# Kernel optimization log

Hardware: AMD Instinct MI355X
Metric: run time of the kernel (lower is better)

Reference implementation:

```python
import jax, jax.numpy as jnp
import numpy as np

TIME_DECAY = 0.1
B, S, D = 2048, 200, 128
H1, H2 = 64, 32


def setup_inputs() -> dict:
    key = jax.random.key(0)
    ks = jax.random.split(key, 8)
    query = jax.random.normal(ks[0], (B, D), dtype=jnp.float32)
    keys = jax.random.normal(ks[1], (B, S, D), dtype=jnp.float32)
    keys_mask = jax.random.randint(ks[2], (B, S), 0, 2).astype(jnp.bool_)
    # Linear weights stored as [in, out] (torch uses [out, in] with x @ W.T; same math)
    W1 = jax.random.normal(ks[3], (4 * D, H1), dtype=jnp.float32) / np.sqrt(4 * D)
    b1 = jnp.zeros((H1,), dtype=jnp.float32)
    a1 = jnp.asarray(0.25, dtype=jnp.float32)  # PReLU default init
    W2 = jax.random.normal(ks[4], (H1, H2), dtype=jnp.float32) / np.sqrt(H1)
    b2 = jnp.zeros((H2,), dtype=jnp.float32)
    a2 = jnp.asarray(0.25, dtype=jnp.float32)
    W3 = jax.random.normal(ks[5], (H2, 1), dtype=jnp.float32) / np.sqrt(H2)
    b3 = jnp.zeros((1,), dtype=jnp.float32)
    return {"query": query, "keys": keys, "keys_mask": keys_mask,
            "W1": W1, "b1": b1, "a1": a1, "W2": W2, "b2": b2, "a2": a2,
            "W3": W3, "b3": b3}


def _prelu(x, a):
    return jnp.maximum(x, 0) + a * jnp.minimum(x, 0)


def reference(query, keys, keys_mask, W1, b1, a1, W2, b2, a2, W3, b3):
    b, s, d = keys.shape
    q = jnp.broadcast_to(query[:, None, :], (b, s, d))
    # [B, S, 4D] concat of feature interactions
    x = jnp.concatenate([keys, q, keys * q, keys - q], axis=-1)
    h = _prelu(x @ W1 + b1, a1)
    h = _prelu(h @ W2 + b2, a2)
    scores = (h @ W3 + b3)[..., 0]  # [B, S]
    pos = jnp.arange(s, dtype=scores.dtype)
    time_w = jnp.exp(TIME_DECAY * (pos - s + 1))  # [S]
    scores = scores * time_w[None, :]
    scores = jnp.where(keys_mask, scores, -jnp.inf)
    w = jax.nn.softmax(scores, axis=-1)
    w = jnp.where(jnp.isnan(w), jnp.zeros_like(w), w)  # all-masked rows -> 0
    weighted_sum = jnp.einsum('bs,bsd->bd', w, keys)
    return weighted_sum, w
```

## Files before the change

### kernel.cpp

```cpp
#include <hip/hip_runtime.h>
#include <math.h>

#define NB 2048
#define NS 200
#define ND 128

typedef __attribute__((ext_vector_type(8))) short bf16x8;
typedef __attribute__((ext_vector_type(4))) float f32x4;
typedef __attribute__((ext_vector_type(4))) unsigned short u16x4;

#define U_W1HI  0
#define U_W1LO  4352
#define U_Q     8704
#define U_BIAS  8832
#define U_B2    8896
#define U_W3    8928
#define U_SC    8960
#define U_WB    9168
#define U_WRED  9376
#define U_BP    9384
#define U_TOTAL 9644

extern "C" __global__ void __launch_bounds__(256, 4)
tdra_main(const float* __restrict__ query,
          const float* __restrict__ keys,
          const int*   __restrict__ kmask,
          const float* __restrict__ W1,
          const float* __restrict__ b1,
          const float* __restrict__ a1p,
          const float* __restrict__ W2,
          const float* __restrict__ b2,
          const float* __restrict__ a2p,
          const float* __restrict__ W3,
          const float* __restrict__ b3p,
          float* __restrict__ out)
{
    __shared__ __align__(16) unsigned int smem[U_TOTAL];
    unsigned short* W1hi = (unsigned short*)(smem + U_W1HI);
    unsigned short* W1lo = (unsigned short*)(smem + U_W1LO);
    float* qf    = (float*)(smem + U_Q);
    float* biasE = (float*)(smem + U_BIAS);
    float* b2f   = (float*)(smem + U_B2);
    float* w3f   = (float*)(smem + U_W3);
    float* scf   = (float*)(smem + U_SC);
    float* wbf   = (float*)(smem + U_WB);
    float* wred  = (float*)(smem + U_WRED);
    float* bpf   = (float*)(smem + U_BP);

    const int tid = threadIdx.x;
    const int b   = blockIdx.x;
    const float a1 = a1p[0];
    const float a2 = a2p[0];
    const float b3 = b3p[0];

    const int wv = tid >> 6;
    const int c  = tid & 15;
    const int G  = (tid >> 4) & 3;

    if (tid < 32) {
        float4 qv = *(const float4*)(query + (size_t)b * ND + tid * 4);
        *(float4*)(qf + tid * 4) = qv;
    } else if (tid < 64) {
        b2f[tid - 32] = b2[tid - 32];
    } else if (tid < 96) {
        w3f[tid - 64] = W3[tid - 64];
    }

    bf16x8 A2h[2][2], A2l[2][2];
    #pragma unroll
    for (int jt = 0; jt < 2; ++jt)
        #pragma unroll
        for (int kt = 0; kt < 2; ++kt)
            #pragma unroll
            for (int e = 0; e < 8; ++e) {
                float x = W2[(kt * 32 + 8 * G + e) * 32 + jt * 16 + c];
                unsigned int u  = __float_as_uint(x);
                unsigned int hb = u & 0xFFFF0000u;
                float lof = x - __uint_as_float(hb);
                A2h[jt][kt][e] = (short)(u >> 16);
                A2l[jt][kt][e] = (short)(__float_as_uint(lof) >> 16);
            }
    __syncthreads();

    {
        int h = tid & 63, dg = tid >> 6;
        #pragma unroll 2
        for (int i = 0; i < 8; ++i) {
            int dblk = dg * 8 + i;
            u16x4 hi4, lo4;
            #pragma unroll
            for (int jj = 0; jj < 4; ++jj) {
                int d = dblk * 4 + jj;
                float qd = qf[d];
                float va = W1[d * 64 + h];
                float vc = W1[16384 + d * 64 + h];
                float vd = W1[24576 + d * 64 + h];
                float x  = va + vd + qd * vc;
                unsigned int u  = __float_as_uint(x);
                unsigned int hb = u & 0xFFFF0000u;
                float lof = x - __uint_as_float(hb);
                hi4[jj] = (unsigned short)(u >> 16);
                lo4[jj] = (unsigned short)(__float_as_uint(lof) >> 16);
            }
            *(u16x4*)(W1hi + h * 136 + dblk * 4) = hi4;
            *(u16x4*)(W1lo + h * 136 + dblk * 4) = lo4;
        }
        int qt = dg;
        const float* pb = W1 + (size_t)(128 + qt * 32) * 64 + h;
        const float* pd = W1 + (size_t)(384 + qt * 32) * 64 + h;
        float p = 0.f;
        #pragma unroll 8
        for (int i = 0; i < 32; ++i)
            p = fmaf(qf[qt * 32 + i], pb[i * 64] - pd[i * 64], p);
        bpf[qt * 65 + h] = p;
    }
    __syncthreads();
    if (tid < 64)
        biasE[tid] = b1[tid] + bpf[tid] + bpf[65 + tid] + bpf[130 + tid] + bpf[195 + tid];
    __syncthreads();

    #pragma unroll 1
    for (int st = wv; st < 13; st += 4) {
        int row = st * 16 + c; if (row > 199) row = 199;
        const float* kp = keys + ((size_t)b * NS + row) * ND + 8 * G;

        bf16x8 B1h[4], B1l[4];
        #pragma unroll
        for (int half = 0; half < 2; ++half) {
            float4 xs[4];
            #pragma unroll
            for (int q_ = 0; q_ < 2; ++q_) {
                xs[2 * q_]     = *(const float4*)(kp + (2 * half + q_) * 32);
                xs[2 * q_ + 1] = *(const float4*)(kp + (2 * half + q_) * 32 + 4);
            }
            #pragma unroll
            for (int q_ = 0; q_ < 2; ++q_) {
                int dt = 2 * half + q_;
                float t_[8] = {xs[2*q_].x, xs[2*q_].y, xs[2*q_].z, xs[2*q_].w,
                               xs[2*q_+1].x, xs[2*q_+1].y, xs[2*q_+1].z, xs[2*q_+1].w};
                #pragma unroll
                for (int e = 0; e < 8; ++e) {
                    unsigned int u  = __float_as_uint(t_[e]);
                    unsigned int hb = u & 0xFFFF0000u;
                    float lof = t_[e] - __uint_as_float(hb);
                    B1h[dt][e] = (short)(u >> 16);
                    B1l[dt][e] = (short)(__float_as_uint(lof) >> 16);
                }
            }
        }

        f32x4 acc1[4];
        #pragma unroll
        for (int ht = 0; ht < 4; ++ht)
            acc1[ht] = *(const f32x4*)(biasE + 16 * ht + 4 * G);
        #pragma unroll
        for (int dt = 0; dt < 4; ++dt) {
            #pragma unroll
            for (int ht = 0; ht < 4; ++ht) {
                int idx = (16 * ht + c) * 136 + 32 * dt + 8 * G;
                bf16x8 A1h = *(const bf16x8*)(W1hi + idx);
                bf16x8 A1l = *(const bf16x8*)(W1lo + idx);
                acc1[ht] = __builtin_amdgcn_mfma_f32_16x16x32_bf16(A1h, B1h[dt], acc1[ht], 0, 0, 0);
                acc1[ht] = __builtin_amdgcn_mfma_f32_16x16x32_bf16(A1h, B1l[dt], acc1[ht], 0, 0, 0);
                acc1[ht] = __builtin_amdgcn_mfma_f32_16x16x32_bf16(A1l, B1h[dt], acc1[ht], 0, 0, 0);
            }
        }

        unsigned int p[4][4];
        #pragma unroll
        for (int ht = 0; ht < 4; ++ht)
            #pragma unroll
            for (int r = 0; r < 4; ++r) {
                float v = acc1[ht][r];
                v = fmaxf(v, 0.f) + a1 * fminf(v, 0.f);
                unsigned int u  = __float_as_uint(v);
                unsigned int hb = u & 0xFFFF0000u;
                float lof = v - __uint_as_float(hb);
                p[ht][r] = (u >> 16) | (__float_as_uint(lof) & 0xFFFF0000u);
            }

        f32x4 acc2[2];
        acc2[0] = *(const f32x4*)(b2f + 4 * G);
        acc2[1] = *(const f32x4*)(b2f + 16 + 4 * G);
        const int srcbase = ((tid & 16) ? 32 : 0) + c;
        #pragma unroll
        for (int kt = 0; kt < 2; ++kt) {
            unsigned int q[8];
            #pragma unroll
            for (int half = 0; half < 2; ++half) {
                int src = srcbase + half * 16;
                #pragma unroll
                for (int r = 0; r < 4; ++r) {
                    unsigned int v0 = (unsigned int)__shfl((int)p[2 * kt][r], src, 64);
                    unsigned int v1 = (unsigned int)__shfl((int)p[2 * kt + 1][r], src, 64);
                    q[half * 4 + r] = (tid & 32) ? v1 : v0;
                }
            }
            bf16x8 B2h_, B2l_;
            #pragma unroll
            for (int e = 0; e < 8; ++e) {
                B2h_[e] = (short)(q[e] & 0xFFFFu);
                B2l_[e] = (short)(q[e] >> 16);
            }
            #pragma unroll
            for (int jt = 0; jt < 2; ++jt) {
                acc2[jt] = __builtin_amdgcn_mfma_f32_16x16x32_bf16(A2h[jt][kt], B2h_, acc2[jt], 0, 0, 0);
                acc2[jt] = __builtin_amdgcn_mfma_f32_16x16x32_bf16(A2h[jt][kt], B2l_, acc2[jt], 0, 0, 0);
                acc2[jt] = __builtin_amdgcn_mfma_f32_16x16x32_bf16(A2l[jt][kt], B2h_, acc2[jt], 0, 0, 0);
            }
        }

        float sv = 0.f;
        #pragma unroll
        for (int jt = 0; jt < 2; ++jt)
            #pragma unroll
            for (int r = 0; r < 4; ++r) {
                float v = acc2[jt][r];
                v = fmaxf(v, 0.f) + a2 * fminf(v, 0.f);
                sv = fmaf(v, w3f[jt * 16 + 4 * G + r], sv);
            }
        sv += __shfl_xor(sv, 16, 64);
        sv += __shfl_xor(sv, 32, 64);
        int srow = st * 16 + c;
        if ((tid & 48) == 0 && srow < NS) scf[srow] = sv + b3;
    }
    __syncthreads();

    float scval = -INFINITY;
    if (tid < NS) {
        if (kmask[(size_t)b * NS + tid] != 0)
            scval = scf[tid] * expf(0.1f * (float)(tid - (NS - 1)));
    }
    const int wid = tid >> 6, lane = tid & 63;
    float mx = scval;
    #pragma unroll
    for (int o = 32; o > 0; o >>= 1) mx = fmaxf(mx, __shfl_xor(mx, o, 64));
    if (lane == 0) wred[wid] = mx;
    __syncthreads();
    float M = fmaxf(fmaxf(wred[0], wred[1]), fmaxf(wred[2], wred[3]));
    float e = (M > -INFINITY) ? expf(scval - M) : 0.f;
    float ssum = e;
    #pragma unroll
    for (int o = 32; o > 0; o >>= 1) ssum += __shfl_xor(ssum, o, 64);
    if (lane == 0) wred[4 + wid] = ssum;
    __syncthreads();
    float SUM = wred[4] + wred[5] + wred[6] + wred[7];
    float wv_ = (SUM > 0.f) ? (e / SUM) : 0.f;
    if (tid < NS) {
        wbf[tid] = wv_;
        out[(size_t)NB * ND + (size_t)b * NS + tid] = wv_;
    }
    __syncthreads();

    {
        const int d = tid & 127, half = tid >> 7;
        const float* kp = keys + ((size_t)b * NS + half * 100) * ND + d;
        float pacc = 0.f;
        #pragma unroll 5
        for (int i = 0; i < 100; ++i)
            pacc = fmaf(wbf[half * 100 + i], kp[(size_t)i * ND], pacc);
        bpf[half * 128 + d] = pacc;
    }
    __syncthreads();
    if (tid < 128)
        out[(size_t)b * ND + tid] = bpf[tid] + bpf[128 + tid];
}

extern "C" void kernel_launch(void* const* d_in, const int* in_sizes, int n_in,
                              void* d_out, int out_size, void* d_ws, size_t ws_size,
                              hipStream_t stream) {
    (void)in_sizes; (void)n_in; (void)d_ws; (void)ws_size; (void)out_size;
    const float* query = (const float*)d_in[0];
    const float* keys  = (const float*)d_in[1];
    const int*   kmask = (const int*)d_in[2];
    const float* W1 = (const float*)d_in[3];
    const float* b1 = (const float*)d_in[4];
    const float* a1 = (const float*)d_in[5];
    const float* W2 = (const float*)d_in[6];
    const float* b2 = (const float*)d_in[7];
    const float* a2 = (const float*)d_in[8];
    const float* W3 = (const float*)d_in[9];
    const float* b3 = (const float*)d_in[10];
    float* out = (float*)d_out;

    hipLaunchKernelGGL(tdra_main, dim3(NB), dim3(256), 0, stream,
                       query, keys, kmask, W1, b1, a1, W2, b2, a2, W3, b3, out);
}
```

Before: 77.36 us.

## Fuse online softmax and weighted sum into the MLP tile loop

Computes the softmax with a running max and sum per thread, in the flash-attention style, and accumulates the weighted key sum from the key values already held in registers. This removes the second pass that reread all keys from global memory, along with the separate reduction barriers. The keys are rebuilt from their hi/lo bf16 split, and partial results are merged with cross-lane shuffles and then across waves. Each thread now keeps 32 extra accumulators, so the launch-bound occupancy hint drops from 4 to 3 blocks. The mask and time-decay factors are also precomputed into shared memory at the start.

Result: slower. 82.51 us (+6.6%).

```diff
diff --git a/kernel.cpp b/kernel.cpp
--- a/kernel.cpp
+++ b/kernel.cpp
@@ -16,12 +16,13 @@
 #define U_B2    8896
 #define U_W3    8928
 #define U_SC    8960
-#define U_WB    9168
-#define U_WRED  9376
-#define U_BP    9384
-#define U_TOTAL 9644
-
-extern "C" __global__ void __launch_bounds__(256, 4)
+#define U_DM    9168
+#define U_O4    9376
+#define U_ML    9888
+#define U_BP    9896
+#define U_TOTAL 10156
+
+extern "C" __global__ void __launch_bounds__(256, 3)
 tdra_main(const float* __restrict__ query,
           const float* __restrict__ keys,
           const int*   __restrict__ kmask,
@@ -43,8 +44,9 @@
     float* b2f   = (float*)(smem + U_B2);
     float* w3f   = (float*)(smem + U_W3);
     float* scf   = (float*)(smem + U_SC);
-    float* wbf   = (float*)(smem + U_WB);
-    float* wred  = (float*)(smem + U_WRED);
+    float* dmf   = (float*)(smem + U_DM);
+    float* o4    = (float*)(smem + U_O4);
+    float* mlf   = (float*)(smem + U_ML);
     float* bpf   = (float*)(smem + U_BP);
 
     const int tid = threadIdx.x;
@@ -64,6 +66,10 @@
         b2f[tid - 32] = b2[tid - 32];
     } else if (tid < 96) {
         w3f[tid - 64] = W3[tid - 64];
+    }
+    if (tid < 208) {
+        int mk = (tid < NS) ? kmask[(size_t)b * NS + tid] : 0;
+        dmf[tid] = mk ? expf(0.1f * (float)(tid - (NS - 1))) : 0.f;
     }
 
     bf16x8 A2h[2][2], A2l[2][2];
@@ -119,10 +125,16 @@
         biasE[tid] = b1[tid] + bpf[tid] + bpf[65 + tid] + bpf[130 + tid] + bpf[195 + tid];
     __syncthreads();
 
+    float m_run = -INFINITY, l_run = 0.f;
+    float o_acc[32];
+    #pragma unroll
+    for (int i = 0; i < 32; ++i) o_acc[i] = 0.f;
+
     #pragma unroll 1
     for (int st = wv; st < 13; st += 4) {
-        int row = st * 16 + c; if (row > 199) row = 199;
-        const float* kp = keys + ((size_t)b * NS + row) * ND + 8 * G;
+        const int rr = st * 16 + c;
+        int row_ld = rr < 199 ? rr : 199;
+        const float* kp = keys + ((size_t)b * NS + row_ld) * ND + 8 * G;
 
         bf16x8 B1h[4], B1l[4];
         #pragma unroll
@@ -221,49 +233,74 @@
             }
         sv += __shfl_xor(sv, 16, 64);
         sv += __shfl_xor(sv, 32, 64);
-        int srow = st * 16 + c;
-        if ((tid & 48) == 0 && srow < NS) scf[srow] = sv + b3;
-    }
+
+        float dm  = dmf[rr];
+        float scm = (dm > 0.f) ? (sv + b3) * dm : -INFINITY;
+        if ((tid & 48) == 0 && rr < NS) scf[rr] = scm;
+
+        if (scm > m_run) {
+            float f = __expf(m_run - scm);
+            l_run *= f;
+            #pragma unroll
+            for (int i = 0; i < 32; ++i) o_acc[i] *= f;
+            m_run = scm;
+        }
+        float wexp = (scm == -INFINITY) ? 0.f : __expf(scm - m_run);
+        l_run += wexp;
+        #pragma unroll
+        for (int dt = 0; dt < 4; ++dt)
+            #pragma unroll
+            for (int e = 0; e < 8; ++e) {
+                float kv = __uint_as_float(((unsigned int)(unsigned short)B1h[dt][e]) << 16)
+                         + __uint_as_float(((unsigned int)(unsigned short)B1l[dt][e]) << 16);
+                o_acc[dt * 8 + e] = fmaf(wexp, kv, o_acc[dt * 8 + e]);
+            }
+    }
+
+    #pragma unroll
+    for (int d_ = 1; d_ < 16; d_ <<= 1) {
+        float mo = __shfl_xor(m_run, d_, 64);
+        float lo = __shfl_xor(l_run, d_, 64);
+        float M2 = fmaxf(m_run, mo);
+        float fs = (m_run == -INFINITY) ? 0.f : __expf(m_run - M2);
+        float fo = (mo    == -INFINITY) ? 0.f : __expf(mo    - M2);
+        l_run = l_run * fs + lo * fo;
+        #pragma unroll
+        for (int i = 0; i < 32; ++i) {
+            float oo = __shfl_xor(o_acc[i], d_, 64);
+            o_acc[i] = o_acc[i] * fs + oo * fo;
+        }
+        m_run = M2;
+    }
+    if ((tid & 15) == 0) {
+        #pragma unroll
+        for (int dt = 0; dt < 4; ++dt) {
+            *(float4*)(o4 + wv * 128 + 32 * dt + 8 * G) =
+                make_float4(o_acc[8*dt+0], o_acc[8*dt+1], o_acc[8*dt+2], o_acc[8*dt+3]);
+            *(float4*)(o4 + wv * 128 + 32 * dt + 8 * G + 4) =
+                make_float4(o_acc[8*dt+4], o_acc[8*dt+5], o_acc[8*dt+6], o_acc[8*dt+7]);
+        }
+    }
+    if ((tid & 63) == 0) { mlf[2 * wv] = m_run; mlf[2 * wv + 1] = l_run; }
     __syncthreads();
 
-    float scval = -INFINITY;
+    float M = fmaxf(fmaxf(mlf[0], mlf[2]), fmaxf(mlf[4], mlf[6]));
+    float fw0 = (mlf[0] == -INFINITY) ? 0.f : __expf(mlf[0] - M);
+    float fw1 = (mlf[2] == -INFINITY) ? 0.f : __expf(mlf[2] - M);
+    float fw2 = (mlf[4] == -INFINITY) ? 0.f : __expf(mlf[4] - M);
+    float fw3 = (mlf[6] == -INFINITY) ? 0.f : __expf(mlf[6] - M);
+    float L = mlf[1] * fw0 + mlf[3] * fw1 + mlf[5] * fw2 + mlf[7] * fw3;
+
+    if (tid < ND) {
+        float od = o4[tid] * fw0 + o4[128 + tid] * fw1
+                 + o4[256 + tid] * fw2 + o4[384 + tid] * fw3;
+        out[(size_t)b * ND + tid] = (L > 0.f) ? od / L : 0.f;
+    }
     if (tid < NS) {
-        if (kmask[(size_t)b * NS + tid] != 0)
-            scval = scf[tid] * expf(0.1f * (float)(tid - (NS - 1)));
-    }
-    const int wid = tid >> 6, lane = tid & 63;
-    float mx = scval;
-    #pragma unroll
-    for (int o = 32; o > 0; o >>= 1) mx = fmaxf(mx, __shfl_xor(mx, o, 64));
-    if (lane == 0) wred[wid] = mx;
-    __syncthreads();
-    float M = fmaxf(fmaxf(wred[0], wred[1]), fmaxf(wred[2], wred[3]));
-    float e = (M > -INFINITY) ? expf(scval - M) : 0.f;
-    float ssum = e;
-    #pragma unroll
-    for (int o = 32; o > 0; o >>= 1) ssum += __shfl_xor(ssum, o, 64);
-    if (lane == 0) wred[4 + wid] = ssum;
-    __syncthreads();
-    float SUM = wred[4] + wred[5] + wred[6] + wred[7];
-    float wv_ = (SUM > 0.f) ? (e / SUM) : 0.f;
-    if (tid < NS) {
-        wbf[tid] = wv_;
+        float s_ = scf[tid];
+        float wv_ = (L > 0.f && s_ > -INFINITY) ? __expf(s_ - M) / L : 0.f;
         out[(size_t)NB * ND + (size_t)b * NS + tid] = wv_;
     }
-    __syncthreads();
-
-    {
-        const int d = tid & 127, half = tid >> 7;
-        const float* kp = keys + ((size_t)b * NS + half * 100) * ND + d;
-        float pacc = 0.f;
-        #pragma unroll 5
-        for (int i = 0; i < 100; ++i)
-            pacc = fmaf(wbf[half * 100 + i], kp[(size_t)i * ND], pacc);
-        bpf[half * 128 + d] = pacc;
-    }
-    __syncthreads();
-    if (tid < 128)
-        out[(size_t)b * ND + tid] = bpf[tid] + bpf[128 + tid];
 }
 
 extern "C" void kernel_launch(void* const* d_in, const int* in_sizes, int n_in,
```

## Prefetch next key tile, pack bf16 splits with perm, vectorize weighted sum

Applied to the files above, without the earlier changes.

The main loop now loads the next 16-row key tile into registers while the current tile goes through the MLP MFMAs, so global loads overlap with compute. The hi/lo bf16 splitting and repacking switch from per-element shifts and inserts to v_perm byte permutes on pairs. The final weighted-sum pass uses float4 loads over 8 row groups with a shared-memory reduction, reusing the W1 smem region for the partial sums. The trade is higher register pressure from the prefetched float4 buffer, which may reduce occupancy under the 4-block launch bound.

After: 107.9 us. +39.5%, slower.

```diff
diff --git a/kernel.cpp b/kernel.cpp
--- a/kernel.cpp
+++ b/kernel.cpp
@@ -7,7 +7,6 @@
 
 typedef __attribute__((ext_vector_type(8))) short bf16x8;
 typedef __attribute__((ext_vector_type(4))) float f32x4;
-typedef __attribute__((ext_vector_type(4))) unsigned short u16x4;
 
 #define U_W1HI  0
 #define U_W1LO  4352
@@ -20,6 +19,15 @@
 #define U_WRED  9376
 #define U_BP    9384
 #define U_TOTAL 9644
+
+union CvtU4 { unsigned int u[4]; bf16x8 v; };
+
+__device__ __forceinline__ unsigned int permhi(unsigned int a, unsigned int b) {
+    return __builtin_amdgcn_perm(a, b, 0x07060302u);
+}
+__device__ __forceinline__ unsigned int permlo(unsigned int a, unsigned int b) {
+    return __builtin_amdgcn_perm(a, b, 0x05040100u);
+}
 
 extern "C" __global__ void __launch_bounds__(256, 4)
 tdra_main(const float* __restrict__ query,
@@ -87,23 +95,22 @@
         #pragma unroll 2
         for (int i = 0; i < 8; ++i) {
             int dblk = dg * 8 + i;
-            u16x4 hi4, lo4;
-            #pragma unroll
-            for (int jj = 0; jj < 4; ++jj) {
-                int d = dblk * 4 + jj;
-                float qd = qf[d];
-                float va = W1[d * 64 + h];
-                float vc = W1[16384 + d * 64 + h];
-                float vd = W1[24576 + d * 64 + h];
-                float x  = va + vd + qd * vc;
-                unsigned int u  = __float_as_uint(x);
-                unsigned int hb = u & 0xFFFF0000u;
-                float lof = x - __uint_as_float(hb);
-                hi4[jj] = (unsigned short)(u >> 16);
-                lo4[jj] = (unsigned short)(__float_as_uint(lof) >> 16);
-            }
-            *(u16x4*)(W1hi + h * 136 + dblk * 4) = hi4;
-            *(u16x4*)(W1lo + h * 136 + dblk * 4) = lo4;
+            unsigned int hp[2], lp[2];
+            #pragma unroll
+            for (int jp = 0; jp < 2; ++jp) {
+                int d0 = dblk * 4 + 2 * jp;
+                float x0 = W1[d0 * 64 + h] + W1[24576 + d0 * 64 + h]
+                         + qf[d0] * W1[16384 + d0 * 64 + h];
+                float x1 = W1[(d0 + 1) * 64 + h] + W1[24576 + (d0 + 1) * 64 + h]
+                         + qf[d0 + 1] * W1[16384 + (d0 + 1) * 64 + h];
+                unsigned int u0 = __float_as_uint(x0), u1 = __float_as_uint(x1);
+                hp[jp] = permhi(u1, u0);
+                float l0 = x0 - __uint_as_float(u0 & 0xFFFF0000u);
+                float l1 = x1 - __uint_as_float(u1 & 0xFFFF0000u);
+                lp[jp] = permhi(__float_as_uint(l1), __float_as_uint(l0));
+            }
+            *(uint2*)(W1hi + h * 136 + dblk * 4) = make_uint2(hp[0], hp[1]);
+            *(uint2*)(W1lo + h * 136 + dblk * 4) = make_uint2(lp[0], lp[1]);
         }
         int qt = dg;
         const float* pb = W1 + (size_t)(128 + qt * 32) * 64 + h;
@@ -119,33 +126,47 @@
         biasE[tid] = b1[tid] + bpf[tid] + bpf[65 + tid] + bpf[130 + tid] + bpf[195 + tid];
     __syncthreads();
 
+    float4 xs[8];
+    {
+        int r0 = wv * 16 + c; if (r0 > 199) r0 = 199;
+        const float* kp = keys + ((size_t)b * NS + r0) * ND + 8 * G;
+        #pragma unroll
+        for (int q_ = 0; q_ < 4; ++q_) {
+            xs[2 * q_]     = *(const float4*)(kp + q_ * 32);
+            xs[2 * q_ + 1] = *(const float4*)(kp + q_ * 32 + 4);
+        }
+    }
+
     #pragma unroll 1
     for (int st = wv; st < 13; st += 4) {
-        int row = st * 16 + c; if (row > 199) row = 199;
-        const float* kp = keys + ((size_t)b * NS + row) * ND + 8 * G;
+        const int rr = st * 16 + c;
 
         bf16x8 B1h[4], B1l[4];
         #pragma unroll
-        for (int half = 0; half < 2; ++half) {
-            float4 xs[4];
-            #pragma unroll
-            for (int q_ = 0; q_ < 2; ++q_) {
-                xs[2 * q_]     = *(const float4*)(kp + (2 * half + q_) * 32);
-                xs[2 * q_ + 1] = *(const float4*)(kp + (2 * half + q_) * 32 + 4);
-            }
-            #pragma unroll
-            for (int q_ = 0; q_ < 2; ++q_) {
-                int dt = 2 * half + q_;
-                float t_[8] = {xs[2*q_].x, xs[2*q_].y, xs[2*q_].z, xs[2*q_].w,
-                               xs[2*q_+1].x, xs[2*q_+1].y, xs[2*q_+1].z, xs[2*q_+1].w};
-                #pragma unroll
-                for (int e = 0; e < 8; ++e) {
-                    unsigned int u  = __float_as_uint(t_[e]);
-                    unsigned int hb = u & 0xFFFF0000u;
-                    float lof = t_[e] - __uint_as_float(hb);
-                    B1h[dt][e] = (short)(u >> 16);
-                    B1l[dt][e] = (short)(__float_as_uint(lof) >> 16);
-                }
+        for (int dt = 0; dt < 4; ++dt) {
+            float fe[8] = {xs[2*dt].x, xs[2*dt].y, xs[2*dt].z, xs[2*dt].w,
+                           xs[2*dt+1].x, xs[2*dt+1].y, xs[2*dt+1].z, xs[2*dt+1].w};
+            CvtU4 H, L;
+            #pragma unroll
+            for (int j = 0; j < 4; ++j) {
+                unsigned int u0 = __float_as_uint(fe[2 * j]);
+                unsigned int u1 = __float_as_uint(fe[2 * j + 1]);
+                H.u[j] = permhi(u1, u0);
+                float l0 = fe[2 * j]     - __uint_as_float(u0 & 0xFFFF0000u);
+                float l1 = fe[2 * j + 1] - __uint_as_float(u1 & 0xFFFF0000u);
+                L.u[j] = permhi(__float_as_uint(l1), __float_as_uint(l0));
+            }
+            B1h[dt] = H.v;
+            B1l[dt] = L.v;
+        }
+
+        if (st + 4 < 13) {
+            int rn = (st + 4) * 16 + c; if (rn > 199) rn = 199;
+            const float* kp = keys + ((size_t)b * NS + rn) * ND + 8 * G;
+            #pragma unroll
+            for (int q_ = 0; q_ < 4; ++q_) {
+                xs[2 * q_]     = *(const float4*)(kp + q_ * 32);
+                xs[2 * q_ + 1] = *(const float4*)(kp + q_ * 32 + 4);
             }
         }
 
@@ -173,10 +194,9 @@
             for (int r = 0; r < 4; ++r) {
                 float v = acc1[ht][r];
                 v = fmaxf(v, 0.f) + a1 * fminf(v, 0.f);
-                unsigned int u  = __float_as_uint(v);
-                unsigned int hb = u & 0xFFFF0000u;
-                float lof = v - __uint_as_float(hb);
-                p[ht][r] = (u >> 16) | (__float_as_uint(lof) & 0xFFFF0000u);
+                unsigned int u = __float_as_uint(v);
+                float lof = v - __uint_as_float(u & 0xFFFF0000u);
+                p[ht][r] = permhi(__float_as_uint(lof), u);
             }
 
         f32x4 acc2[2];
@@ -196,17 +216,17 @@
                     q[half * 4 + r] = (tid & 32) ? v1 : v0;
                 }
             }
-            bf16x8 B2h_, B2l_;
-            #pragma unroll
-            for (int e = 0; e < 8; ++e) {
-                B2h_[e] = (short)(q[e] & 0xFFFFu);
-                B2l_[e] = (short)(q[e] >> 16);
+            CvtU4 BH, BL;
+            #pragma unroll
+            for (int j = 0; j < 4; ++j) {
+                BH.u[j] = permlo(q[2 * j + 1], q[2 * j]);
+                BL.u[j] = permhi(q[2 * j + 1], q[2 * j]);
             }
             #pragma unroll
             for (int jt = 0; jt < 2; ++jt) {
-                acc2[jt] = __builtin_amdgcn_mfma_f32_16x16x32_bf16(A2h[jt][kt], B2h_, acc2[jt], 0, 0, 0);
-                acc2[jt] = __builtin_amdgcn_mfma_f32_16x16x32_bf16(A2h[jt][kt], B2l_, acc2[jt], 0, 0, 0);
-                acc2[jt] = __builtin_amdgcn_mfma_f32_16x16x32_bf16(A2l[jt][kt], B2h_, acc2[jt], 0, 0, 0);
+                acc2[jt] = __builtin_amdgcn_mfma_f32_16x16x32_bf16(A2h[jt][kt], BH.v, acc2[jt], 0, 0, 0);
+                acc2[jt] = __builtin_amdgcn_mfma_f32_16x16x32_bf16(A2h[jt][kt], BL.v, acc2[jt], 0, 0, 0);
+                acc2[jt] = __builtin_amdgcn_mfma_f32_16x16x32_bf16(A2l[jt][kt], BH.v, acc2[jt], 0, 0, 0);
             }
         }
 
@@ -221,8 +241,7 @@
             }
         sv += __shfl_xor(sv, 16, 64);
         sv += __shfl_xor(sv, 32, 64);
-        int srow = st * 16 + c;
-        if ((tid & 48) == 0 && srow < NS) scf[srow] = sv + b3;
+        if ((tid & 48) == 0 && rr < NS) scf[rr] = sv + b3;
     }
     __syncthreads();
 
@@ -252,18 +271,29 @@
     }
     __syncthreads();
 
+    float* part = (float*)(smem + U_W1HI);
     {
-        const int d = tid & 127, half = tid >> 7;
-        const float* kp = keys + ((size_t)b * NS + half * 100) * ND + d;
-        float pacc = 0.f;
+        const int dq = tid & 31, sg = tid >> 5;
+        const float* kp = keys + ((size_t)b * NS + sg * 25) * ND + dq * 4;
+        float ax = 0.f, ay = 0.f, az = 0.f, aw = 0.f;
         #pragma unroll 5
-        for (int i = 0; i < 100; ++i)
-            pacc = fmaf(wbf[half * 100 + i], kp[(size_t)i * ND], pacc);
-        bpf[half * 128 + d] = pacc;
-    }
-    __syncthreads();
-    if (tid < 128)
-        out[(size_t)b * ND + tid] = bpf[tid] + bpf[128 + tid];
+        for (int i = 0; i < 25; ++i) {
+            float ww = wbf[sg * 25 + i];
+            float4 kv = *(const float4*)(kp + (size_t)i * ND);
+            ax = fmaf(ww, kv.x, ax);
+            ay = fmaf(ww, kv.y, ay);
+            az = fmaf(ww, kv.z, az);
+            aw = fmaf(ww, kv.w, aw);
+        }
+        *(float4*)(part + sg * 128 + dq * 4) = make_float4(ax, ay, az, aw);
+    }
+    __syncthreads();
+    if (tid < 128) {
+        float s = 0.f;
+        #pragma unroll
+        for (int g = 0; g < 8; ++g) s += part[g * 128 + tid];
+        out[(size_t)b * ND + tid] = s;
+    }
 }
 
 extern "C" void kernel_launch(void* const* d_in, const int* in_sizes, int n_in,
```

## Use five waves per block and vectorize weighted-sum reduction across row groups

Applied to the files above, without the earlier changes.

Raises the block from four to five wavefronts, so the 13 MLP row tiles are spread over five waves, and rebalances the W1 folding and the softmax reductions to match. The final weighted sum now uses float4 key loads with ten row-groups of 20 rows each, reducing partials through shared memory that reuses the W1 region. The aim is a shorter critical path per block and better load vectorization, at the cost of higher register and LDS pressure under the new launch bounds, which may lower occupancy.

New measurement: 93.23 us. +20.5%, slower.

```diff
diff --git a/kernel.cpp b/kernel.cpp
--- a/kernel.cpp
+++ b/kernel.cpp
@@ -18,10 +18,10 @@
 #define U_SC    8960
 #define U_WB    9168
 #define U_WRED  9376
-#define U_BP    9384
-#define U_TOTAL 9644
-
-extern "C" __global__ void __launch_bounds__(256, 4)
+#define U_BP    9392
+#define U_TOTAL 9652
+
+extern "C" __global__ void __launch_bounds__(320, 5)
 tdra_main(const float* __restrict__ query,
           const float* __restrict__ keys,
           const int*   __restrict__ kmask,
@@ -84,9 +84,8 @@
 
     {
         int h = tid & 63, dg = tid >> 6;
-        #pragma unroll 2
-        for (int i = 0; i < 8; ++i) {
-            int dblk = dg * 8 + i;
+        #pragma unroll 1
+        for (int dblk = dg; dblk < 32; dblk += 5) {
             u16x4 hi4, lo4;
             #pragma unroll
             for (int jj = 0; jj < 4; ++jj) {
@@ -105,14 +104,16 @@
             *(u16x4*)(W1hi + h * 136 + dblk * 4) = hi4;
             *(u16x4*)(W1lo + h * 136 + dblk * 4) = lo4;
         }
-        int qt = dg;
-        const float* pb = W1 + (size_t)(128 + qt * 32) * 64 + h;
-        const float* pd = W1 + (size_t)(384 + qt * 32) * 64 + h;
-        float p = 0.f;
-        #pragma unroll 8
-        for (int i = 0; i < 32; ++i)
-            p = fmaf(qf[qt * 32 + i], pb[i * 64] - pd[i * 64], p);
-        bpf[qt * 65 + h] = p;
+        if (dg < 4) {
+            int qt = dg;
+            const float* pb = W1 + (size_t)(128 + qt * 32) * 64 + h;
+            const float* pd = W1 + (size_t)(384 + qt * 32) * 64 + h;
+            float p = 0.f;
+            #pragma unroll 8
+            for (int i = 0; i < 32; ++i)
+                p = fmaf(qf[qt * 32 + i], pb[i * 64] - pd[i * 64], p);
+            bpf[qt * 65 + h] = p;
+        }
     }
     __syncthreads();
     if (tid < 64)
@@ -120,9 +121,10 @@
     __syncthreads();
 
     #pragma unroll 1
-    for (int st = wv; st < 13; st += 4) {
-        int row = st * 16 + c; if (row > 199) row = 199;
-        const float* kp = keys + ((size_t)b * NS + row) * ND + 8 * G;
+    for (int st = wv; st < 13; st += 5) {
+        const int rr = st * 16 + c;
+        int row_ld = rr < 199 ? rr : 199;
+        const float* kp = keys + ((size_t)b * NS + row_ld) * ND + 8 * G;
 
         bf16x8 B1h[4], B1l[4];
         #pragma unroll
@@ -136,13 +138,13 @@
             #pragma unroll
             for (int q_ = 0; q_ < 2; ++q_) {
                 int dt = 2 * half + q_;
-                float t_[8] = {xs[2*q_].x, xs[2*q_].y, xs[2*q_].z, xs[2*q_].w,
+                float fe[8] = {xs[2*q_].x, xs[2*q_].y, xs[2*q_].z, xs[2*q_].w,
                                xs[2*q_+1].x, xs[2*q_+1].y, xs[2*q_+1].z, xs[2*q_+1].w};
                 #pragma unroll
                 for (int e = 0; e < 8; ++e) {
-                    unsigned int u  = __float_as_uint(t_[e]);
+                    unsigned int u  = __float_as_uint(fe[e]);
                     unsigned int hb = u & 0xFFFF0000u;
-                    float lof = t_[e] - __uint_as_float(hb);
+                    float lof = fe[e] - __uint_as_float(hb);
                     B1h[dt][e] = (short)(u >> 16);
                     B1l[dt][e] = (short)(__float_as_uint(lof) >> 16);
                 }
@@ -221,8 +223,7 @@
             }
         sv += __shfl_xor(sv, 16, 64);
         sv += __shfl_xor(sv, 32, 64);
-        int srow = st * 16 + c;
-        if ((tid & 48) == 0 && srow < NS) scf[srow] = sv + b3;
+        if ((tid & 48) == 0 && rr < NS) scf[rr] = sv + b3;
     }
     __syncthreads();
 
@@ -237,14 +238,18 @@
     for (int o = 32; o > 0; o >>= 1) mx = fmaxf(mx, __shfl_xor(mx, o, 64));
     if (lane == 0) wred[wid] = mx;
     __syncthreads();
-    float M = fmaxf(fmaxf(wred[0], wred[1]), fmaxf(wred[2], wred[3]));
-    float e = (M > -INFINITY) ? expf(scval - M) : 0.f;
+    float M = wred[0];
+    #pragma unroll
+    for (int g = 1; g < 5; ++g) M = fmaxf(M, wred[g]);
+    float e = (M > -INFINITY && scval > -INFINITY) ? expf(scval - M) : 0.f;
     float ssum = e;
     #pragma unroll
     for (int o = 32; o > 0; o >>= 1) ssum += __shfl_xor(ssum, o, 64);
-    if (lane == 0) wred[4 + wid] = ssum;
-    __syncthreads();
-    float SUM = wred[4] + wred[5] + wred[6] + wred[7];
+    if (lane == 0) wred[8 + wid] = ssum;
+    __syncthreads();
+    float SUM = 0.f;
+    #pragma unroll
+    for (int g = 0; g < 5; ++g) SUM += wred[8 + g];
     float wv_ = (SUM > 0.f) ? (e / SUM) : 0.f;
     if (tid < NS) {
         wbf[tid] = wv_;
@@ -252,18 +257,29 @@
     }
     __syncthreads();
 
+    float* part = (float*)(smem + U_W1HI);
     {
-        const int d = tid & 127, half = tid >> 7;
-        const float* kp = keys + ((size_t)b * NS + half * 100) * ND + d;
-        float pacc = 0.f;
+        const int dq = tid & 31, sg = tid >> 5;
+        const float* kp = keys + ((size_t)b * NS + sg * 20) * ND + dq * 4;
+        float ax = 0.f, ay = 0.f, az = 0.f, aw = 0.f;
         #pragma unroll 5
-        for (int i = 0; i < 100; ++i)
-            pacc = fmaf(wbf[half * 100 + i], kp[(size_t)i * ND], pacc);
-        bpf[half * 128 + d] = pacc;
-    }
-    __syncthreads();
-    if (tid < 128)
-        out[(size_t)b * ND + tid] = bpf[tid] + bpf[128 + tid];
+        for (int i = 0; i < 20; ++i) {
+            float ww = wbf[sg * 20 + i];
+            float4 kv = *(const float4*)(kp + (size_t)i * ND);
+            ax = fmaf(ww, kv.x, ax);
+            ay = fmaf(ww, kv.y, ay);
+            az = fmaf(ww, kv.z, az);
+            aw = fmaf(ww, kv.w, aw);
+        }
+        *(float4*)(part + sg * 128 + dq * 4) = make_float4(ax, ay, az, aw);
+    }
+    __syncthreads();
+    if (tid < 128) {
+        float s = 0.f;
+        #pragma unroll
+        for (int g = 0; g < 10; ++g) s += part[g * 128 + tid];
+        out[(size_t)b * ND + tid] = s;
+    }
 }
 
 extern "C" void kernel_launch(void* const* d_in, const int* in_sizes, int n_in,
@@ -283,6 +299,6 @@
     const float* b3 = (const float*)d_in[10];
     float* out = (float*)d_out;
 
-    hipLaunchKernelGGL(tdra_main, dim3(NB), dim3(256), 0, stream,
+    hipLaunchKernelGGL(tdra_main, dim3(NB), dim3(320), 0, stream,
                        query, keys, kmask, W1, b1, a1, W2, b2, a2, W3, b3, out);
 }
```
